# Optimization experiments

Measured on AMD Instinct MI355X. Metric: run time of the kernel, lower is better.

The kernel has to match this reference:

```python
import jax, jax.numpy as jnp
import numpy as np

N = 8192
D_IN = 512
D_OUT = 64
ALPHA = 0.2  # LeakyReLU negative slope
NEG_BIG = -9e15


def setup_inputs() -> dict:
    key = jax.random.key(0)
    k1, k2, k3, k4 = jax.random.split(key, 4)
    h = jax.random.normal(k1, (N, D_IN), dtype=jnp.float32)
    mask = (jax.random.uniform(k2, (N, N)) < 0.05).astype(jnp.float32)
    lamda = jnp.float32(0.5)
    # xavier_uniform(gain=1.414) approximated with scaled normals
    W = jax.random.normal(k3, (D_IN, D_OUT), dtype=jnp.float32) * (1.414 * np.sqrt(2.0 / (D_IN + D_OUT)))
    a = jax.random.normal(k4, (2 * D_OUT, 1), dtype=jnp.float32) * (1.414 * np.sqrt(2.0 / (2 * D_OUT + 1)))
    return {"h": h, "mask": mask, "lamda": lamda, "W": W, "a": a}


def reference(h, mask, lamda, W, a):
    f_out = W.shape[1]
    Wh = h @ W                                  # [N, F]
    Wh1 = Wh @ a[:f_out, :]                     # [N, 1]
    Wh2 = Wh @ a[f_out:, :]                     # [N, 1]
    e = Wh1 + Wh2.T                             # [N, N]
    e = jnp.where(e > 0, e, ALPHA * e)          # LeakyReLU
    # dischange is initialized to zeros in the source, so the mask-update
    # wheres use a zero tensor (broadcast scalar here to avoid an NxN alloc).
    dischange0 = jnp.float32(0.0)
    attention = jnp.where(mask > 0, e, NEG_BIG)
    new_mask = jnp.where(dischange0 > lamda, jnp.float32(1.0), mask)
    new_mask = jnp.where(dischange0 < -lamda, jnp.float32(0.0), new_mask)
    attention = jnp.where(new_mask > 0, e, NEG_BIG)
    attention = jax.nn.softmax(attention, axis=1)
    # F.dropout with training=False (eval / reference mode) is identity.
    out = attention @ Wh                        # [N, F]
    return jax.nn.elu(out)                      # concat=True branch
```

## Files before the change

kernel.cpp:

```cpp
#include <hip/hip_runtime.h>

#define N_NODES 8192
#define D_IN 512
#define D_OUT 64
#define LRELU_ALPHA 0.2f
#define KSPLIT 8
#define KSLICE (N_NODES / KSPLIT)
#define NCHUNK (KSLICE / 64)

typedef __attribute__((ext_vector_type(8))) short bf16x8;
typedef __attribute__((ext_vector_type(4))) float f32x4;

__device__ __forceinline__ unsigned short f2bf(float x) {
    unsigned u = __float_as_uint(x);
    u += 0x7fffu + ((u >> 16) & 1u);
    return (unsigned short)(u >> 16);
}

__device__ __forceinline__ float pgate(float mk, float w2v, float wh1v, float& lsum) {
    float e = wh1v + w2v;
    e = fmaxf(e, LRELU_ALPHA * e);
    float p = mk * __expf(e);
    lsum += p;
    return p;
}

__global__ __launch_bounds__(256) void k_gemm(const float* __restrict__ h,
                                              const float* __restrict__ W,
                                              const float* __restrict__ a,
                                              unsigned short* __restrict__ WhTp3,
                                              float* __restrict__ Wh1,
                                              float* __restrict__ Wh2) {
    __shared__ float hs[32][68];
    __shared__ float Ws[64][64];
    const int tid = threadIdx.x;
    const int r0 = blockIdx.x * 32;
    const int tf = tid & 15;
    const int tr = tid >> 4;
    float acc[2][4] = {{0.f,0.f,0.f,0.f},{0.f,0.f,0.f,0.f}};

    for (int kc = 0; kc < D_IN; kc += 64) {
        {
            int rr = tid >> 4;
            int cc = (tid & 15) * 4;
            float4 v0 = *(const float4*)&h[(size_t)(r0 + rr) * D_IN + kc + cc];
            float4 v1 = *(const float4*)&h[(size_t)(r0 + rr + 16) * D_IN + kc + cc];
            *(float4*)&hs[rr][cc] = v0;
            *(float4*)&hs[rr + 16][cc] = v1;
        }
        #pragma unroll
        for (int p = 0; p < 4; ++p) {
            int kk = (tid >> 4) + p * 16;
            int cc = (tid & 15) * 4;
            *(float4*)&Ws[kk][cc] = *(const float4*)&W[(size_t)(kc + kk) * D_OUT + cc];
        }
        __syncthreads();
        #pragma unroll
        for (int k = 0; k < 64; k += 4) {
            float4 a0 = *(const float4*)&hs[tr*2][k];
            float4 a1 = *(const float4*)&hs[tr*2+1][k];
            float av0[4] = {a0.x, a0.y, a0.z, a0.w};
            float av1[4] = {a1.x, a1.y, a1.z, a1.w};
            #pragma unroll
            for (int kk = 0; kk < 4; ++kk) {
                float4 b = *(const float4*)&Ws[k+kk][tf*4];
                acc[0][0] += av0[kk]*b.x; acc[0][1] += av0[kk]*b.y;
                acc[0][2] += av0[kk]*b.z; acc[0][3] += av0[kk]*b.w;
                acc[1][0] += av1[kk]*b.x; acc[1][1] += av1[kk]*b.y;
                acc[1][2] += av1[kk]*b.z; acc[1][3] += av1[kk]*b.w;
            }
        }
        __syncthreads();
    }
    const int orow = r0 + tr*2;

    {
        const int cc  = orow >> 6;
        const int cw  = orow & 63;
        const int hh  = cw >> 5;
        const int rem = cw & 31;
        const int jhi = rem >> 4;
        const int gg  = (rem >> 2) & 3;
        const int jlo = cw & 3;
        const int j   = jhi * 4 + jlo;
        #pragma unroll
        for (int k = 0; k < 4; ++k) {
            const int f = tf * 4 + k;
            const int L = gg * 16 + (f & 15);
            const int s = (2 * (f >> 4) + hh) ^ (L & 7);
            const size_t sidx = ((size_t)(cc * 64 + L) * 8 + s) * 8 + j;
            unsigned v = (unsigned)f2bf(acc[0][k]) | ((unsigned)f2bf(acc[1][k]) << 16);
            *(unsigned*)&WhTp3[sidx] = v;
        }
    }

    float a1v[4], a2v[4];
    #pragma unroll
    for (int k = 0; k < 4; ++k) { a1v[k] = a[tf*4 + k]; a2v[k] = a[64 + tf*4 + k]; }
    float s1 = 0.f, t1 = 0.f, s2 = 0.f, t2 = 0.f;
    #pragma unroll
    for (int k = 0; k < 4; ++k) {
        s1 += acc[0][k] * a1v[k];
        t1 += acc[1][k] * a1v[k];
        s2 += acc[0][k] * a2v[k];
        t2 += acc[1][k] * a2v[k];
    }
    #pragma unroll
    for (int d = 1; d < 16; d <<= 1) {
        s1 += __shfl_xor(s1, d);
        t1 += __shfl_xor(t1, d);
        s2 += __shfl_xor(s2, d);
        t2 += __shfl_xor(t2, d);
    }
    if (tf == 0) {
        Wh1[orow] = s1; Wh1[orow + 1] = t1;
        Wh2[orow] = s2; Wh2[orow + 1] = t2;
    }
}

__global__ __launch_bounds__(512, 4) void k_fused(const float* __restrict__ mask,
                                                  const unsigned short* __restrict__ WhTp3,
                                                  const float* __restrict__ Wh1,
                                                  const float* __restrict__ Wh2,
                                                  float* __restrict__ pacc,
                                                  float* __restrict__ plsum) {
    __shared__ unsigned short bbuf[2][4096];
    __shared__ float wh2lds[KSLICE];

    const int tid  = threadIdx.x;
    const int wave = tid >> 6;
    const int lane = tid & 63;
    const int i16 = lane & 15;
    const int g   = lane >> 4;
    const int rg    = blockIdx.x >> 3;
    const int slice = blockIdx.x & 7;
    const int Rw    = rg * 128 + wave * 16;
    const int ccbase = slice * NCHUNK;

    const float wh1v = Wh1[Rw + i16];
    const float* mrow = mask + (size_t)(Rw + i16) * N_NODES + slice * KSLICE;

    if (tid < 256) {
        *(float4*)&wh2lds[tid * 4] = *(const float4*)&Wh2[ccbase * 64 + tid * 4];
    }

    f32x4 acc0 = {0.f,0.f,0.f,0.f}, acc1 = {0.f,0.f,0.f,0.f};
    f32x4 acc2 = {0.f,0.f,0.f,0.f}, acc3 = {0.f,0.f,0.f,0.f};
    float lsum = 0.f;

#define STAGE(c, par)                                                                   \
    {                                                                                   \
        const unsigned short* src = WhTp3 + ((size_t)(ccbase + (c)) * 512 + wave * 64 + lane) * 8; \
        __builtin_amdgcn_global_load_lds(src, &bbuf[par][wave * 512], 16, 0, 0);        \
    }

    STAGE(0, 0);
    __syncthreads();

    #pragma unroll 2
    for (int c = 0; c < NCHUNK; ++c) {
        const int par = c & 1;

        const float* mp = mrow + c * 64 + g * 4;
        const float4 M0 = *(const float4*)(mp);
        const float4 M1 = *(const float4*)(mp + 16);
        const float4 M2 = *(const float4*)(mp + 32);
        const float4 M3 = *(const float4*)(mp + 48);

        if (c + 1 < NCHUNK) STAGE(c + 1, par ^ 1);
        __builtin_amdgcn_sched_barrier(0);

        const float* wp = &wh2lds[c * 64 + g * 4];
        const float4 W0 = *(const float4*)(wp);
        const float4 W1 = *(const float4*)(wp + 16);
        const float4 W2 = *(const float4*)(wp + 32);
        const float4 W3 = *(const float4*)(wp + 48);

        const unsigned short* lb = &bbuf[par][lane * 64];
        const bf16x8 B00 = *(const bf16x8*)(lb + ((0 ^ (lane & 7)) * 8));
        const bf16x8 B01 = *(const bf16x8*)(lb + ((1 ^ (lane & 7)) * 8));
        const bf16x8 B10 = *(const bf16x8*)(lb + ((2 ^ (lane & 7)) * 8));
        const bf16x8 B11 = *(const bf16x8*)(lb + ((3 ^ (lane & 7)) * 8));
        const bf16x8 B20 = *(const bf16x8*)(lb + ((4 ^ (lane & 7)) * 8));
        const bf16x8 B21 = *(const bf16x8*)(lb + ((5 ^ (lane & 7)) * 8));
        const bf16x8 B30 = *(const bf16x8*)(lb + ((6 ^ (lane & 7)) * 8));
        const bf16x8 B31 = *(const bf16x8*)(lb + ((7 ^ (lane & 7)) * 8));

        bf16x8 af0, af1;
        af0[0] = (short)f2bf(pgate(M0.x, W0.x, wh1v, lsum));
        af0[1] = (short)f2bf(pgate(M0.y, W0.y, wh1v, lsum));
        af0[2] = (short)f2bf(pgate(M0.z, W0.z, wh1v, lsum));
        af0[3] = (short)f2bf(pgate(M0.w, W0.w, wh1v, lsum));
        af0[4] = (short)f2bf(pgate(M1.x, W1.x, wh1v, lsum));
        af0[5] = (short)f2bf(pgate(M1.y, W1.y, wh1v, lsum));
        af0[6] = (short)f2bf(pgate(M1.z, W1.z, wh1v, lsum));
        af0[7] = (short)f2bf(pgate(M1.w, W1.w, wh1v, lsum));
        af1[0] = (short)f2bf(pgate(M2.x, W2.x, wh1v, lsum));
        af1[1] = (short)f2bf(pgate(M2.y, W2.y, wh1v, lsum));
        af1[2] = (short)f2bf(pgate(M2.z, W2.z, wh1v, lsum));
        af1[3] = (short)f2bf(pgate(M2.w, W2.w, wh1v, lsum));
        af1[4] = (short)f2bf(pgate(M3.x, W3.x, wh1v, lsum));
        af1[5] = (short)f2bf(pgate(M3.y, W3.y, wh1v, lsum));
        af1[6] = (short)f2bf(pgate(M3.z, W3.z, wh1v, lsum));
        af1[7] = (short)f2bf(pgate(M3.w, W3.w, wh1v, lsum));

        acc0 = __builtin_amdgcn_mfma_f32_16x16x32_bf16(af0, B00, acc0, 0, 0, 0);
        acc1 = __builtin_amdgcn_mfma_f32_16x16x32_bf16(af0, B10, acc1, 0, 0, 0);
        acc2 = __builtin_amdgcn_mfma_f32_16x16x32_bf16(af0, B20, acc2, 0, 0, 0);
        acc3 = __builtin_amdgcn_mfma_f32_16x16x32_bf16(af0, B30, acc3, 0, 0, 0);
        acc0 = __builtin_amdgcn_mfma_f32_16x16x32_bf16(af1, B01, acc0, 0, 0, 0);
        acc1 = __builtin_amdgcn_mfma_f32_16x16x32_bf16(af1, B11, acc1, 0, 0, 0);
        acc2 = __builtin_amdgcn_mfma_f32_16x16x32_bf16(af1, B21, acc2, 0, 0, 0);
        acc3 = __builtin_amdgcn_mfma_f32_16x16x32_bf16(af1, B31, acc3, 0, 0, 0);

        if (c + 1 < NCHUNK) __syncthreads();
    }
#undef STAGE

    lsum += __shfl_xor(lsum, 16);
    lsum += __shfl_xor(lsum, 32);

    #pragma unroll
    for (int r = 0; r < 4; ++r) {
        const int row = Rw + g * 4 + r;
        float* pr = pacc + ((size_t)slice * N_NODES + row) * D_OUT + i16;
        pr[ 0] = acc0[r];
        pr[16] = acc1[r];
        pr[32] = acc2[r];
        pr[48] = acc3[r];
    }
    if (lane < 16) plsum[(size_t)slice * N_NODES + Rw + lane] = lsum;
}

__global__ __launch_bounds__(256) void k_finish(const float* __restrict__ pacc,
                                                const float* __restrict__ plsum,
                                                float* __restrict__ out) {
    const int idx = blockIdx.x * 256 + threadIdx.x;
    const int row = idx >> 4;
    const int tf4 = (idx & 15) * 4;
    float4 s = {0.f, 0.f, 0.f, 0.f};
    float L = 0.f;
    #pragma unroll
    for (int k = 0; k < KSPLIT; ++k) {
        float4 v = *(const float4*)&pacc[((size_t)k * N_NODES + row) * D_OUT + tf4];
        s.x += v.x; s.y += v.y; s.z += v.z; s.w += v.w;
        L += plsum[(size_t)k * N_NODES + row];
    }
    const float inv = (L > 0.f) ? 1.f / L : 0.f;
    float4 o;
    o.x = s.x * inv; o.y = s.y * inv; o.z = s.z * inv; o.w = s.w * inv;
    o.x = (o.x > 0.f) ? o.x : (__expf(o.x) - 1.f);
    o.y = (o.y > 0.f) ? o.y : (__expf(o.y) - 1.f);
    o.z = (o.z > 0.f) ? o.z : (__expf(o.z) - 1.f);
    o.w = (o.w > 0.f) ? o.w : (__expf(o.w) - 1.f);
    *(float4*)&out[(size_t)row * D_OUT + tf4] = o;
}

extern "C" void kernel_launch(void* const* d_in, const int* in_sizes, int n_in,
                              void* d_out, int out_size, void* d_ws, size_t ws_size,
                              hipStream_t stream) {
    const float* h    = (const float*)d_in[0];
    const float* mask = (const float*)d_in[1];
    const float* W    = (const float*)d_in[3];
    const float* a    = (const float*)d_in[4];
    float* out = (float*)d_out;

    unsigned short* WhTp3 = (unsigned short*)d_ws;
    float* Wh1 = (float*)((char*)d_ws + (size_t)D_OUT * N_NODES * sizeof(unsigned short));
    float* Wh2 = Wh1 + N_NODES;
    float* pacc = Wh2 + N_NODES;
    float* plsum = pacc + (size_t)KSPLIT * N_NODES * D_OUT;

    k_gemm<<<N_NODES / 32, 256, 0, stream>>>(h, W, a, WhTp3, Wh1, Wh2);
    k_fused<<<(N_NODES / 128) * KSPLIT, 512, 0, stream>>>(mask, WhTp3, Wh1, Wh2, pacc, plsum);
    k_finish<<<(N_NODES * D_OUT / 4) / 256, 256, 0, stream>>>(pacc, plsum, out);
}
```

Before: 86.44 us.

## Stage mask tiles into LDS via async global_load_lds with swizzle, single-buffered

```diff
diff --git a/kernel.cpp b/kernel.cpp
--- a/kernel.cpp
+++ b/kernel.cpp
@@ -124,7 +124,8 @@
                                                   const float* __restrict__ Wh2,
                                                   float* __restrict__ pacc,
                                                   float* __restrict__ plsum) {
-    __shared__ unsigned short bbuf[2][4096];
+    __shared__ float mbuf[8][16][64];
+    __shared__ unsigned short bbuf[4096];
     __shared__ float wh2lds[KSLICE];
 
     const int tid  = threadIdx.x;
@@ -138,7 +139,7 @@
     const int ccbase = slice * NCHUNK;
 
     const float wh1v = Wh1[Rw + i16];
-    const float* mrow = mask + (size_t)(Rw + i16) * N_NODES + slice * KSLICE;
+    const float* mstrip = mask + (size_t)Rw * N_NODES + slice * KSLICE;
 
     if (tid < 256) {
         *(float4*)&wh2lds[tid * 4] = *(const float4*)&Wh2[ccbase * 64 + tid * 4];
@@ -148,35 +149,34 @@
     f32x4 acc2 = {0.f,0.f,0.f,0.f}, acc3 = {0.f,0.f,0.f,0.f};
     float lsum = 0.f;
 
-#define STAGE(c, par)                                                                   \
-    {                                                                                   \
-        const unsigned short* src = WhTp3 + ((size_t)(ccbase + (c)) * 512 + wave * 64 + lane) * 8; \
-        __builtin_amdgcn_global_load_lds(src, &bbuf[par][wave * 512], 16, 0, 0);        \
-    }
-
-    STAGE(0, 0);
-    __syncthreads();
+#define GDMA(c)                                                                          \
+    {                                                                                    \
+        const float* ms_ = mstrip + (c) * 64;                                            \
+        const float* s0_ = ms_ + (size_t)(0  + g) * N_NODES + ((i16 ^ ((0  + g) & 7)) << 2); \
+        const float* s1_ = ms_ + (size_t)(4  + g) * N_NODES + ((i16 ^ ((4  + g) & 7)) << 2); \
+        const float* s2_ = ms_ + (size_t)(8  + g) * N_NODES + ((i16 ^ ((8  + g) & 7)) << 2); \
+        const float* s3_ = ms_ + (size_t)(12 + g) * N_NODES + ((i16 ^ ((12 + g) & 7)) << 2); \
+        __builtin_amdgcn_global_load_lds(s0_, &mbuf[wave][ 0][0], 16, 0, 0);             \
+        __builtin_amdgcn_global_load_lds(s1_, &mbuf[wave][ 4][0], 16, 0, 0);             \
+        __builtin_amdgcn_global_load_lds(s2_, &mbuf[wave][ 8][0], 16, 0, 0);             \
+        __builtin_amdgcn_global_load_lds(s3_, &mbuf[wave][12][0], 16, 0, 0);             \
+        const unsigned short* sb_ = WhTp3 + ((size_t)(ccbase + (c)) * 512 + wave * 64 + lane) * 8; \
+        __builtin_amdgcn_global_load_lds(sb_, &bbuf[wave * 512], 16, 0, 0);              \
+    }
+
+    GDMA(0);
 
     #pragma unroll 2
     for (int c = 0; c < NCHUNK; ++c) {
-        const int par = c & 1;
-
-        const float* mp = mrow + c * 64 + g * 4;
-        const float4 M0 = *(const float4*)(mp);
-        const float4 M1 = *(const float4*)(mp + 16);
-        const float4 M2 = *(const float4*)(mp + 32);
-        const float4 M3 = *(const float4*)(mp + 48);
-
-        if (c + 1 < NCHUNK) STAGE(c + 1, par ^ 1);
-        __builtin_amdgcn_sched_barrier(0);
-
-        const float* wp = &wh2lds[c * 64 + g * 4];
-        const float4 W0 = *(const float4*)(wp);
-        const float4 W1 = *(const float4*)(wp + 16);
-        const float4 W2 = *(const float4*)(wp + 32);
-        const float4 W3 = *(const float4*)(wp + 48);
-
-        const unsigned short* lb = &bbuf[par][lane * 64];
+        __syncthreads();
+
+        const int sw = i16 & 7;
+        const float4 M0 = *(const float4*)&mbuf[wave][i16][((0*4 + g) ^ sw) << 2];
+        const float4 M1 = *(const float4*)&mbuf[wave][i16][((1*4 + g) ^ sw) << 2];
+        const float4 M2 = *(const float4*)&mbuf[wave][i16][((2*4 + g) ^ sw) << 2];
+        const float4 M3 = *(const float4*)&mbuf[wave][i16][((3*4 + g) ^ sw) << 2];
+
+        const unsigned short* lb = &bbuf[lane * 64];
         const bf16x8 B00 = *(const bf16x8*)(lb + ((0 ^ (lane & 7)) * 8));
         const bf16x8 B01 = *(const bf16x8*)(lb + ((1 ^ (lane & 7)) * 8));
         const bf16x8 B10 = *(const bf16x8*)(lb + ((2 ^ (lane & 7)) * 8));
@@ -185,6 +185,17 @@
         const bf16x8 B21 = *(const bf16x8*)(lb + ((5 ^ (lane & 7)) * 8));
         const bf16x8 B30 = *(const bf16x8*)(lb + ((6 ^ (lane & 7)) * 8));
         const bf16x8 B31 = *(const bf16x8*)(lb + ((7 ^ (lane & 7)) * 8));
+
+        const float* wp = &wh2lds[c * 64 + g * 4];
+        const float4 W0 = *(const float4*)(wp);
+        const float4 W1 = *(const float4*)(wp + 16);
+        const float4 W2 = *(const float4*)(wp + 32);
+        const float4 W3 = *(const float4*)(wp + 48);
+
+        __syncthreads();
+
+        if (c + 1 < NCHUNK) GDMA(c + 1);
+        __builtin_amdgcn_sched_barrier(0);
 
         bf16x8 af0, af1;
         af0[0] = (short)f2bf(pgate(M0.x, W0.x, wh1v, lsum));
@@ -212,10 +223,8 @@
         acc1 = __builtin_amdgcn_mfma_f32_16x16x32_bf16(af1, B11, acc1, 0, 0, 0);
         acc2 = __builtin_amdgcn_mfma_f32_16x16x32_bf16(af1, B21, acc2, 0, 0, 0);
         acc3 = __builtin_amdgcn_mfma_f32_16x16x32_bf16(af1, B31, acc3, 0, 0, 0);
-
-        if (c + 1 < NCHUNK) __syncthreads();
-    }
-#undef STAGE
+    }
+#undef GDMA
 
     lsum += __shfl_xor(lsum, 16);
     lsum += __shfl_xor(lsum, 32);
```

Measured after the change: 120.1 us. 1.39x slower.
